# Performance work log

Measured on AMD Instinct MI355X. Metric: run time of the kernel, lower is better.

Reference implementation:

```python
import jax, jax.numpy as jnp
import numpy as np

N = 100000       # nodes
E = 1600000      # edges (avg degree 16)
D_IN = 128
D_HID = 32
D_OUT = 32
H = 4            # heads
NEG_SLOPE = 0.2  # GATConv default leaky_relu slope


def setup_inputs() -> dict:
    key = jax.random.key(0)
    ks = jax.random.split(key, 10)
    s = 0.1
    return {
        "edge": jax.random.randint(ks[0], (2, E), 0, N),
        "features": jax.random.normal(ks[1], (N, D_IN), jnp.float32),
        # layer 1 params: W [in, H*hid], attention vectors per head [H, hid]
        "W1": jax.random.normal(ks[2], (D_IN, H * D_HID), jnp.float32) * s,
        "a1_src": jax.random.normal(ks[3], (H, D_HID), jnp.float32) * s,
        "a1_dst": jax.random.normal(ks[4], (H, D_HID), jnp.float32) * s,
        "b1": jnp.zeros((H * D_HID,), jnp.float32),
        # layer 2 params
        "W2": jax.random.normal(ks[5], (H * D_HID, H * D_OUT), jnp.float32) * s,
        "a2_src": jax.random.normal(ks[6], (H, D_OUT), jnp.float32) * s,
        "a2_dst": jax.random.normal(ks[7], (H, D_OUT), jnp.float32) * s,
        "b2": jnp.zeros((H * D_OUT,), jnp.float32),
    }


def gat_conv(x, src, dst, W, a_src, a_dst, b, heads, d_out):
    """Multi-head GAT layer, concat heads. x: [N, d_in] -> [N, heads*d_out]."""
    n = x.shape[0]
    h = (x @ W).reshape(n, heads, d_out)                 # [N,H,D]
    e_src = jnp.einsum('nhd,hd->nh', h, a_src)           # [N,H]
    e_dst = jnp.einsum('nhd,hd->nh', h, a_dst)           # [N,H]
    e = jax.nn.leaky_relu(e_src[src] + e_dst[dst], NEG_SLOPE)  # [E,H]
    # softmax over incoming edges of each dst node (stable via segment max)
    m = jax.lax.stop_gradient(jax.ops.segment_max(e, dst, num_segments=n))
    w = jnp.exp(e - m[dst])                              # [E,H]
    den = jax.ops.segment_sum(w, dst, num_segments=n)    # [N,H]
    alpha = w / den[dst]                                 # [E,H]
    out = jax.ops.segment_sum(alpha[:, :, None] * h[src], dst, num_segments=n)
    return out.reshape(n, heads * d_out) + b


def reference(edge, features, W1, a1_src, a1_dst, b1, W2, a2_src, a2_dst, b2):
    src, dst = edge[0], edge[1]
    h = jax.nn.relu(gat_conv(features, src, dst, W1, a1_src, a1_dst, b1, H, D_HID))
    h = gat_conv(h, src, dst, W2, a2_src, a2_dst, b2, H, D_OUT)
    return jax.nn.log_softmax(h, axis=1)
```

## Files before the change

### kernel.cpp

```cpp
#include <hip/hip_runtime.h>
#include <hip/hip_bf16.h>
#include <math.h>

#define N_NODES 100000
#define N_EDGES 1600000
#define NHEADS 4
#define NEG_SLOPE 0.2f
#define NSUP 196
#define SSHIFT 9
#define SMASK 511
#define CHUNK 4096
#define NBLK ((N_EDGES + CHUNK - 1) / CHUNK)
#define LCAP 72
#define NBANK 8
#define BCAP2 1200
#define SCAP (NBANK * BCAP2)
#define CPAD 16

typedef __attribute__((ext_vector_type(8))) short short8;
typedef __attribute__((ext_vector_type(4))) float f32x4;
typedef __attribute__((ext_vector_type(2))) float f32x2;

__device__ __forceinline__ unsigned short f2bf(float f) {
    unsigned int u = __float_as_uint(f);
    u += 0x7fffu + ((u >> 16) & 1u);
    return (unsigned short)(u >> 16);
}
__device__ __forceinline__ f32x2 bfpair(unsigned int u) {
    f32x2 r;
    r.x = __uint_as_float(u << 16);
    r.y = __uint_as_float(u & 0xffff0000u);
    return r;
}
__device__ __forceinline__ short8 pack8(float4 f0, float4 f1) {
    short8 v;
    v[0] = (short)f2bf(f0.x); v[1] = (short)f2bf(f0.y);
    v[2] = (short)f2bf(f0.z); v[3] = (short)f2bf(f0.w);
    v[4] = (short)f2bf(f1.x); v[5] = (short)f2bf(f1.y);
    v[6] = (short)f2bf(f1.z); v[7] = (short)f2bf(f1.w);
    return v;
}

__global__ void pack_w_kernel(const float* __restrict__ W1,
                              const float* __restrict__ a1s,
                              const float* __restrict__ a1d,
                              const float* __restrict__ W2,
                              const float* __restrict__ a2s,
                              const float* __restrict__ a2d,
                              unsigned short* __restrict__ Wp1,
                              unsigned short* __restrict__ Wp2,
                              int* __restrict__ cursors) {
    if (blockIdx.x >= 144) {
        for (int i = threadIdx.x; i < NSUP * NBANK * CPAD; i += 256)
            cursors[i] = 0;
        return;
    }
    const int which = blockIdx.x >= 72;
    const float* W      = which ? W2 : W1;
    const float* a_src  = which ? a2s : a1s;
    const float* a_dst  = which ? a2d : a1d;
    unsigned short* Wp  = which ? Wp2 : Wp1;
    int idx = (blockIdx.x - (which ? 72 : 0)) * 256 + threadIdx.x;
    int j    = idx & 7;
    int lane = (idx >> 3) & 63;
    int kc   = (idx >> 9) & 3;
    int ct   = idx >> 11;
    int k = kc * 32 + ((lane >> 4) & 3) * 8 + j;
    int n = lane & 15;
    float v = 0.f;
    if (ct < 8) {
        v = W[k * 128 + ct * 16 + n];
    } else if (n < 8) {
        int hd = n & 3;
        const float* av = (n < 4 ? a_src : a_dst) + hd * 32;
        const float* wr = W + k * 128 + hd * 32;
#pragma unroll
        for (int t = 0; t < 32; ++t) v = fmaf(wr[t], av[t], v);
    }
    Wp[idx] = f2bf(v);
}

template <bool XF32>
__global__ __launch_bounds__(256) void gemm_mfma_kernel(
        const void* __restrict__ xv,
        const unsigned short* __restrict__ Wp,
        unsigned short* __restrict__ h, float* __restrict__ esd, int n_rows) {
    __shared__ unsigned short Wl[18432];

    const int t = threadIdx.x;
    {
        const uint4* s4 = (const uint4*)Wp;
        uint4* d4 = (uint4*)Wl;
#pragma unroll
        for (int p = 0; p < 9; ++p) d4[p * 256 + t] = s4[p * 256 + t];
    }
    __syncthreads();

    const int lane = t & 63, wave = t >> 6;
    const int l15 = lane & 15, quad = lane >> 4;
    const int rbase = blockIdx.x * 128 + wave * 32;

    short8 a[2][4];
#pragma unroll
    for (int rt = 0; rt < 2; ++rt) {
        int r = rbase + rt * 16 + l15;
        r = r < n_rows ? r : n_rows - 1;
        if (XF32) {
            const float* xr = (const float*)xv + (size_t)r * 128 + quad * 8;
#pragma unroll
            for (int kc = 0; kc < 4; ++kc) {
                float4 f0 = *(const float4*)(xr + kc * 32);
                float4 f1 = *(const float4*)(xr + kc * 32 + 4);
                a[rt][kc] = pack8(f0, f1);
            }
        } else {
            const unsigned short* xr =
                (const unsigned short*)xv + (size_t)r * 128 + quad * 8;
#pragma unroll
            for (int kc = 0; kc < 4; ++kc)
                a[rt][kc] = *(const short8*)(xr + kc * 32);
        }
    }

    f32x4 acc[2][9];
#pragma unroll
    for (int rt = 0; rt < 2; ++rt)
#pragma unroll
        for (int ct = 0; ct < 9; ++ct)
            acc[rt][ct] = (f32x4){0.f, 0.f, 0.f, 0.f};

#pragma unroll
    for (int ct = 0; ct < 9; ++ct) {
#pragma unroll
        for (int kc = 0; kc < 4; ++kc) {
            short8 b = *(const short8*)&Wl[((ct * 4 + kc) * 64 + lane) * 8];
            acc[0][ct] = __builtin_amdgcn_mfma_f32_16x16x32_bf16(
                a[0][kc], b, acc[0][ct], 0, 0, 0);
            acc[1][ct] = __builtin_amdgcn_mfma_f32_16x16x32_bf16(
                a[1][kc], b, acc[1][ct], 0, 0, 0);
        }
    }

#pragma unroll
    for (int rt = 0; rt < 2; ++rt) {
#pragma unroll
        for (int i = 0; i < 4; ++i) {
            int r = rbase + rt * 16 + quad * 4 + i;
            if (r < n_rows) {
                unsigned short* hp = h + (size_t)r * 128 + l15;
#pragma unroll
                for (int ct = 0; ct < 8; ++ct)
                    hp[ct * 16] = f2bf(acc[rt][ct][i]);
                if (l15 < 8) esd[r * 8 + l15] = acc[rt][8][i];
            }
        }
    }
}

__global__ __launch_bounds__(256) void scatter_kernel(
        const int* __restrict__ src, const int* __restrict__ dst,
        int* __restrict__ cursors, unsigned int* __restrict__ sslab) {
    __shared__ unsigned int lists[NSUP * LCAP];
    __shared__ int lcnt[NSUP];
    __shared__ int posb[NSUP];
    const int t = threadIdx.x;
    for (int i = t; i < NSUP; i += 256) lcnt[i] = 0;
    __syncthreads();
    const int bank = blockIdx.x & (NBANK - 1);
    const int e0 = blockIdx.x * CHUNK;
#pragma unroll
    for (int k = 0; k < 4; ++k) {
        int e4 = e0 + (k * 256 + t) * 4;
        if (e4 + 3 < N_EDGES) {
            int4 d4 = *(const int4*)(dst + e4);
            int4 s4 = *(const int4*)(src + e4);
            int dd[4] = {d4.x, d4.y, d4.z, d4.w};
            int ss[4] = {s4.x, s4.y, s4.z, s4.w};
#pragma unroll
            for (int j = 0; j < 4; ++j) {
                int su = dd[j] >> SSHIFT;
                int pos = atomicAdd(&lcnt[su], 1);
                if (pos < LCAP)
                    lists[su * LCAP + pos] =
                        (unsigned)ss[j] | ((unsigned)(dd[j] & SMASK) << 17);
            }
        } else {
            for (int j = 0; j < 4; ++j) {
                int e = e4 + j;
                if (e < N_EDGES) {
                    int d = dst[e];
                    int su = d >> SSHIFT;
                    int pos = atomicAdd(&lcnt[su], 1);
                    if (pos < LCAP)
                        lists[su * LCAP + pos] =
                            (unsigned)src[e] | ((unsigned)(d & SMASK) << 17);
                }
            }
        }
    }
    __syncthreads();
    if (t < NSUP) {
        int n = lcnt[t]; n = n > LCAP ? LCAP : n;
        int p = atomicAdd(&cursors[(t * NBANK + bank) * CPAD], n);
        int room = BCAP2 - p; if (room < 0) room = 0;
        if (n > room) n = room;
        posb[t] = p; lcnt[t] = n;
    }
    __syncthreads();
    const int lane = t & 63, wave = t >> 6;
    for (int s = wave; s < NSUP; s += 4) {
        int n = lcnt[s];
        unsigned int* dstp = sslab + (size_t)s * SCAP + bank * BCAP2 + posb[s];
        for (int i = lane; i < n; i += 64) dstp[i] = lists[s * LCAP + i];
    }
}

__global__ __launch_bounds__(512) void super_build_kernel(
        const unsigned int* __restrict__ sslab, const int* __restrict__ cursors,
        int* __restrict__ rowptr, int* __restrict__ csr_src) {
    __shared__ int hist[512];
    __shared__ int ws[8];
    __shared__ int lo_sh;
    const int s = blockIdx.x;
    const int t = threadIdx.x, lane = t & 63, wave = t >> 6;

    {
        int val = 0, v = 0;
        if (t < 256) {
            if (t < NSUP) {
#pragma unroll
                for (int k = 0; k < NBANK; ++k) {
                    int c = cursors[(t * NBANK + k) * CPAD];
                    val += c > BCAP2 ? BCAP2 : c;
                }
            }
            v = val;
#pragma unroll
            for (int off = 1; off < 64; off <<= 1) {
                int u = __shfl_up(v, off);
                if (lane >= off) v += u;
            }
            if (lane == 63) ws[wave] = v;
        }
        __syncthreads();
        if (t < 256) {
            int woff = 0, tot = 0;
#pragma unroll
            for (int w = 0; w < 4; ++w) { if (w < wave) woff += ws[w]; tot += ws[w]; }
            if (t == s) lo_sh = woff + v - val;
            if (s == 0 && t == 0) rowptr[N_NODES] = tot;
        }
        __syncthreads();
    }
    const int lo = lo_sh;

    int cnt[NBANK];
#pragma unroll
    for (int k = 0; k < NBANK; ++k) {
        int c = cursors[(s * NBANK + k) * CPAD];
        cnt[k] = c > BCAP2 ? BCAP2 : c;
    }
    const unsigned int* sp = sslab + (size_t)s * SCAP;
    hist[t] = 0;
    __syncthreads();
#pragma unroll
    for (int k = 0; k < NBANK; ++k)
        for (int i = t; i < cnt[k]; i += 512)
            atomicAdd(&hist[sp[k * BCAP2 + i] >> 17], 1);
    __syncthreads();
    int val = hist[t];
    int v = val;
#pragma unroll
    for (int off = 1; off < 64; off <<= 1) {
        int u = __shfl_up(v, off);
        if (lane >= off) v += u;
    }
    if (lane == 63) ws[wave] = v;
    __syncthreads();
    int woff = 0;
#pragma unroll
    for (int w = 0; w < 8; ++w) if (w < wave) woff += ws[w];
    int excl = woff + v - val;
    hist[t] = lo + excl;
    int node = s * 512 + t;
    if (node < N_NODES) rowptr[node] = lo + excl;
    __syncthreads();
#pragma unroll
    for (int k = 0; k < NBANK; ++k)
        for (int i = t; i < cnt[k]; i += 512) {
            unsigned int rec = sp[k * BCAP2 + i];
            int loc = rec >> 17;
            int pos = atomicAdd(&hist[loc], 1);
            csr_src[pos] = (int)(rec & 0x1FFFFu);
        }
}

template <bool LOGSOFTMAX>
__global__ __launch_bounds__(256) void aggregate_kernel(
        const int* __restrict__ csr_src, const int* __restrict__ rowptr,
        const float* __restrict__ esd,
        const unsigned short* __restrict__ hb, const float* __restrict__ b,
        void* __restrict__ out) {
    const int lane = threadIdx.x & 63;
    const int wave = threadIdx.x >> 6;
    const int n = blockIdx.x * 4 + wave;
    if (n >= N_NODES) return;
    const int eo = lane >> 4;
    const int cl = lane & 15;
    const int c0 = cl * 8;
    const int hd = cl >> 2;
    const float edn = esd[n * 8 + 4 + hd];
    const int base = rowptr[n];
    const int dg = rowptr[n + 1] - base;

    f32x2 acc2[4];
#pragma unroll
    for (int j = 0; j < 4; ++j) acc2[j] = (f32x2){0.f, 0.f};
    float wsum = 0.f;

    if (dg > 0) {
        const int myidx = csr_src[base + (lane < dg ? lane : dg - 1)];
        const int nit = (dg + 3) >> 2;
        const unsigned hbo = (unsigned)c0 * 2u;
        const unsigned edo = (unsigned)hd * 4u;
        const char* hbp = (const char*)hb;
        const char* esp = (const char*)esd;

        auto getS = [&](int j) -> int {
            int o = 4 * j + eo;
            if (4 * j < 64) return __shfl(myidx, o);
            int oc = o < dg ? o : dg - 1;
            return csr_src[base + oc];
        };
        auto loadP = [&](int s) -> uint4 {
            return *(const uint4*)(hbp + (((unsigned)s << 8) + hbo));
        };
        auto loadE = [&](int s, int j) -> float {
            float e = *(const float*)(esp + (((unsigned)s << 5) + edo));
            return (4 * j + eo < dg) ? e : -1e30f;
        };

        int s0 = getS(0);
        uint4 p0 = loadP(s0);
        float e0 = loadE(s0, 0);
        uint4 p1 = p0; float e1 = e0;
        if (nit > 1) {
            int s1 = getS(1);
            p1 = loadP(s1);
            e1 = loadE(s1, 1);
        }
#pragma unroll 2
        for (int j = 0; j < nit; ++j) {
            uint4 p2 = p1; float e2 = e1;
            if (j + 2 < nit) {
                int s2 = getS(j + 2);
                p2 = loadP(s2);
                e2 = loadE(s2, j + 2);
            }
            float sc = e0 + edn;
            sc = sc > 0.f ? sc : NEG_SLOPE * sc;
            float w = __expf(sc);
            f32x2 wv = {w, w};
            acc2[0] = __builtin_elementwise_fma(wv, bfpair(p0.x), acc2[0]);
            acc2[1] = __builtin_elementwise_fma(wv, bfpair(p0.y), acc2[1]);
            acc2[2] = __builtin_elementwise_fma(wv, bfpair(p0.z), acc2[2]);
            acc2[3] = __builtin_elementwise_fma(wv, bfpair(p0.w), acc2[3]);
            wsum += w;
            p0 = p1; e0 = e1; p1 = p2; e1 = e2;
        }
    }

    float acc[8];
#pragma unroll
    for (int j = 0; j < 4; ++j) {
        acc[2 * j]     = acc2[j].x;
        acc[2 * j + 1] = acc2[j].y;
    }

#pragma unroll
    for (int j = 0; j < 8; ++j) {
        acc[j] += __shfl_xor(acc[j], 16);
        acc[j] += __shfl_xor(acc[j], 32);
    }
    wsum += __shfl_xor(wsum, 16);
    wsum += __shfl_xor(wsum, 32);

    float inv = wsum > 0.f ? 1.f / wsum : 0.f;
    float bl[8];
    *(float4*)&bl[0] = *(const float4*)(b + c0);
    *(float4*)&bl[4] = *(const float4*)(b + c0 + 4);
    float v[8];
#pragma unroll
    for (int j = 0; j < 8; ++j) v[j] = acc[j] * inv + bl[j];

    if (!LOGSOFTMAX) {
        if (lane < 16) {
            unsigned int pk[4];
#pragma unroll
            for (int j = 0; j < 4; ++j) {
                float r0 = v[2 * j]     > 0.f ? v[2 * j]     : 0.f;
                float r1 = v[2 * j + 1] > 0.f ? v[2 * j + 1] : 0.f;
                pk[j] = (unsigned int)f2bf(r0) | ((unsigned int)f2bf(r1) << 16);
            }
            *(uint4*)((unsigned short*)out + (size_t)n * 128 + c0) =
                make_uint4(pk[0], pk[1], pk[2], pk[3]);
        }
    } else {
        float m = v[0];
#pragma unroll
        for (int j = 1; j < 8; ++j) m = fmaxf(m, v[j]);
#pragma unroll
        for (int s = 1; s < 16; s <<= 1) m = fmaxf(m, __shfl_xor(m, s));
        float se = 0.f;
#pragma unroll
        for (int j = 0; j < 8; ++j) se += __expf(v[j] - m);
#pragma unroll
        for (int s = 1; s < 16; s <<= 1) se += __shfl_xor(se, s);
        float ls = m + logf(se);
        if (lane < 16) {
            float* o = (float*)out + (size_t)n * 128 + c0;
            *(float4*)o = make_float4(v[0] - ls, v[1] - ls, v[2] - ls, v[3] - ls);
            *(float4*)(o + 4) = make_float4(v[4] - ls, v[5] - ls, v[6] - ls, v[7] - ls);
        }
    }
}

extern "C" void kernel_launch(void* const* d_in, const int* in_sizes, int n_in,
                              void* d_out, int out_size, void* d_ws, size_t ws_size,
                              hipStream_t stream) {
    const int*   edge = (const int*)d_in[0];
    const int*   src  = edge;
    const int*   dst  = edge + N_EDGES;
    const float* feat = (const float*)d_in[1];
    const float* W1   = (const float*)d_in[2];
    const float* a1s  = (const float*)d_in[3];
    const float* a1d  = (const float*)d_in[4];
    const float* b1   = (const float*)d_in[5];
    const float* W2   = (const float*)d_in[6];
    const float* a2s  = (const float*)d_in[7];
    const float* a2d  = (const float*)d_in[8];
    const float* b2   = (const float*)d_in[9];
    float* out = (float*)d_out;

    unsigned short* hb  = (unsigned short*)d_ws;
    unsigned short* x1b = hb + (size_t)N_NODES * 128;
    unsigned short* Wp1 = x1b + (size_t)N_NODES * 128;
    unsigned short* Wp2 = Wp1 + 18432;
    float* esd = (float*)(Wp2 + 18432);
    int* rowptr   = (int*)(esd + (size_t)N_NODES * 8);
    int* cursors  = rowptr + (N_NODES + 1);
    unsigned int* sslab = (unsigned int*)(cursors + NSUP * NBANK * CPAD);
    int* csr_src  = (int*)(sslab + (size_t)NSUP * SCAP);

    const int gemm_blk  = (N_NODES + 127) / 128;
    const int agg_blk   = (N_NODES + 3) / 4;

    pack_w_kernel<<<145, 256, 0, stream>>>(W1, a1s, a1d, W2, a2s, a2d,
                                           Wp1, Wp2, cursors);

    scatter_kernel<<<NBLK, 256, 0, stream>>>(src, dst, cursors, sslab);
    super_build_kernel<<<NSUP, 512, 0, stream>>>(sslab, cursors, rowptr, csr_src);

    gemm_mfma_kernel<true><<<gemm_blk, 256, 0, stream>>>(feat, Wp1, hb, esd, N_NODES);
    aggregate_kernel<false><<<agg_blk, 256, 0, stream>>>(
        csr_src, rowptr, esd, hb, b1, x1b);

    gemm_mfma_kernel<false><<<gemm_blk, 256, 0, stream>>>(x1b, Wp2, hb, esd, N_NODES);
    aggregate_kernel<true><<<agg_blk, 256, 0, stream>>>(
        csr_src, rowptr, esd, hb, b2, out);
}
```

Before: 330.8 us.

## Merge layer-1 GEMM and edge scatter into one heterogeneous launch

Folds the layer-1 feature GEMM and the edge bucketing scatter into a single kernel whose blocks branch on blockIdx: the first 782 blocks do the GEMM, the rest do the scatter, sharing one shared-memory buffer. The goal is to remove one launch and let the compute-bound GEMM overlap with the memory/atomic-bound scatter. LCAP drops from 72 to 56 so the scatter's shared footprint fits the shared buffer sized for the GEMM's weights. That raises the chance of per-superblock list overflow, which is silently clamped and could drop edges.

```diff
diff --git a/kernel.cpp b/kernel.cpp
--- a/kernel.cpp
+++ b/kernel.cpp
@@ -11,11 +11,13 @@
 #define SMASK 511
 #define CHUNK 4096
 #define NBLK ((N_EDGES + CHUNK - 1) / CHUNK)
-#define LCAP 72
+#define LCAP 56
 #define NBANK 8
 #define BCAP2 1200
 #define SCAP (NBANK * BCAP2)
 #define CPAD 16
+#define GEMM_BLK 782
+#define FUSED_SMEM 45472
 
 typedef __attribute__((ext_vector_type(8))) short short8;
 typedef __attribute__((ext_vector_type(4))) float f32x4;
@@ -81,12 +83,10 @@
 }
 
 template <bool XF32>
-__global__ __launch_bounds__(256) void gemm_mfma_kernel(
-        const void* __restrict__ xv,
-        const unsigned short* __restrict__ Wp,
-        unsigned short* __restrict__ h, float* __restrict__ esd, int n_rows) {
-    __shared__ unsigned short Wl[18432];
-
+__device__ __forceinline__ void gemm_body(
+        const void* __restrict__ xv, const unsigned short* __restrict__ Wp,
+        unsigned short* __restrict__ h, float* __restrict__ esd,
+        unsigned short* Wl, int bid) {
     const int t = threadIdx.x;
     {
         const uint4* s4 = (const uint4*)Wp;
@@ -98,13 +98,13 @@
 
     const int lane = t & 63, wave = t >> 6;
     const int l15 = lane & 15, quad = lane >> 4;
-    const int rbase = blockIdx.x * 128 + wave * 32;
+    const int rbase = bid * 128 + wave * 32;
 
     short8 a[2][4];
 #pragma unroll
     for (int rt = 0; rt < 2; ++rt) {
         int r = rbase + rt * 16 + l15;
-        r = r < n_rows ? r : n_rows - 1;
+        r = r < N_NODES ? r : N_NODES - 1;
         if (XF32) {
             const float* xr = (const float*)xv + (size_t)r * 128 + quad * 8;
 #pragma unroll
@@ -146,7 +146,7 @@
 #pragma unroll
         for (int i = 0; i < 4; ++i) {
             int r = rbase + rt * 16 + quad * 4 + i;
-            if (r < n_rows) {
+            if (r < N_NODES) {
                 unsigned short* hp = h + (size_t)r * 128 + l15;
 #pragma unroll
                 for (int ct = 0; ct < 8; ++ct)
@@ -157,17 +157,18 @@
     }
 }
 
-__global__ __launch_bounds__(256) void scatter_kernel(
+__device__ __forceinline__ void scatter_body(
         const int* __restrict__ src, const int* __restrict__ dst,
-        int* __restrict__ cursors, unsigned int* __restrict__ sslab) {
-    __shared__ unsigned int lists[NSUP * LCAP];
-    __shared__ int lcnt[NSUP];
-    __shared__ int posb[NSUP];
+        int* __restrict__ cursors, unsigned int* __restrict__ sslab,
+        unsigned char* smem, int sbid) {
+    unsigned int* lists = (unsigned int*)smem;
+    int* lcnt = (int*)(smem + NSUP * LCAP * 4);
+    int* posb = lcnt + NSUP;
     const int t = threadIdx.x;
     for (int i = t; i < NSUP; i += 256) lcnt[i] = 0;
     __syncthreads();
-    const int bank = blockIdx.x & (NBANK - 1);
-    const int e0 = blockIdx.x * CHUNK;
+    const int bank = sbid & (NBANK - 1);
+    const int e0 = sbid * CHUNK;
 #pragma unroll
     for (int k = 0; k < 4; ++k) {
         int e4 = e0 + (k * 256 + t) * 4;
@@ -213,6 +214,27 @@
         unsigned int* dstp = sslab + (size_t)s * SCAP + bank * BCAP2 + posb[s];
         for (int i = lane; i < n; i += 64) dstp[i] = lists[s * LCAP + i];
     }
+}
+
+__global__ __launch_bounds__(256) void gemm1_scatter_kernel(
+        const float* __restrict__ feat, const unsigned short* __restrict__ Wp1,
+        unsigned short* __restrict__ hb, float* __restrict__ esd,
+        const int* __restrict__ src, const int* __restrict__ dst,
+        int* __restrict__ cursors, unsigned int* __restrict__ sslab) {
+    __shared__ __align__(16) unsigned char smem[FUSED_SMEM];
+    if (blockIdx.x < GEMM_BLK) {
+        gemm_body<true>(feat, Wp1, hb, esd, (unsigned short*)smem, blockIdx.x);
+    } else {
+        scatter_body(src, dst, cursors, sslab, smem, blockIdx.x - GEMM_BLK);
+    }
+}
+
+__global__ __launch_bounds__(256) void gemm_mfma_kernel(
+        const unsigned short* __restrict__ x,
+        const unsigned short* __restrict__ Wp,
+        unsigned short* __restrict__ h, float* __restrict__ esd) {
+    __shared__ __align__(16) unsigned short Wl[18432];
+    gemm_body<false>(x, Wp, h, esd, Wl, blockIdx.x);
 }
 
 __global__ __launch_bounds__(512) void super_build_kernel(
@@ -452,20 +474,20 @@
     unsigned int* sslab = (unsigned int*)(cursors + NSUP * NBANK * CPAD);
     int* csr_src  = (int*)(sslab + (size_t)NSUP * SCAP);
 
-    const int gemm_blk  = (N_NODES + 127) / 128;
-    const int agg_blk   = (N_NODES + 3) / 4;
+    const int agg_blk = (N_NODES + 3) / 4;
 
     pack_w_kernel<<<145, 256, 0, stream>>>(W1, a1s, a1d, W2, a2s, a2d,
                                            Wp1, Wp2, cursors);
 
-    scatter_kernel<<<NBLK, 256, 0, stream>>>(src, dst, cursors, sslab);
+    gemm1_scatter_kernel<<<GEMM_BLK + NBLK, 256, 0, stream>>>(
+        feat, Wp1, hb, esd, src, dst, cursors, sslab);
+
     super_build_kernel<<<NSUP, 512, 0, stream>>>(sslab, cursors, rowptr, csr_src);
 
-    gemm_mfma_kernel<true><<<gemm_blk, 256, 0, stream>>>(feat, Wp1, hb, esd, N_NODES);
     aggregate_kernel<false><<<agg_blk, 256, 0, stream>>>(
         csr_src, rowptr, esd, hb, b1, x1b);
 
-    gemm_mfma_kernel<false><<<gemm_blk, 256, 0, stream>>>(x1b, Wp2, hb, esd, N_NODES);
+    gemm_mfma_kernel<<<GEMM_BLK, 256, 0, stream>>>(x1b, Wp2, hb, esd);
     aggregate_kernel<true><<<agg_blk, 256, 0, stream>>>(
         csr_src, rowptr, esd, hb, b2, out);
 }
```

New measurement: 327.9 us. No clear change (-0.9%).
